# Kernel tuning notes

Measured on AMD Instinct MI355X. Metric: run time of the kernel, lower is better.

The kernel has to match this reference:

```python
import jax, jax.numpy as jnp
import numpy as np
import math

C = 512
TEXT_DIM = 768
HEADS = 8
HEAD_DIM = C // HEADS
GROUPS = 32
EPS = 1e-5


def setup_inputs() -> dict:
    key = jax.random.key(0)
    ks = jax.random.split(key, 12)
    B, H, W, T = 16, 64, 64, 77
    s = lambda fan_in: 1.0 / math.sqrt(fan_in)
    return {
        "x": jax.random.normal(ks[0], (B, C, H, W), jnp.float32),
        "text_emb": jax.random.normal(ks[1], (B, T, TEXT_DIM), jnp.float32),
        "gn_gamma": jnp.ones((C,), jnp.float32),
        "gn_beta": jnp.zeros((C,), jnp.float32),
        "q_w": jax.random.uniform(ks[2], (C, C), jnp.float32, -s(C), s(C)),
        "q_b": jax.random.uniform(ks[3], (C,), jnp.float32, -s(C), s(C)),
        "k_w": jax.random.uniform(ks[4], (C, TEXT_DIM), jnp.float32, -s(TEXT_DIM), s(TEXT_DIM)),
        "k_b": jax.random.uniform(ks[5], (C,), jnp.float32, -s(TEXT_DIM), s(TEXT_DIM)),
        "v_w": jax.random.uniform(ks[6], (C, TEXT_DIM), jnp.float32, -s(TEXT_DIM), s(TEXT_DIM)),
        "v_b": jax.random.uniform(ks[7], (C,), jnp.float32, -s(TEXT_DIM), s(TEXT_DIM)),
        "proj_w": jax.random.uniform(ks[8], (C, C), jnp.float32, -s(C), s(C)),
        "proj_b": jax.random.uniform(ks[9], (C,), jnp.float32, -s(C), s(C)),
    }


def _group_norm(x, gamma, beta):
    b, c, h, w = x.shape
    xg = x.reshape(b, GROUPS, c // GROUPS, h, w)
    mu = jnp.mean(xg, axis=(2, 3, 4), keepdims=True)
    var = jnp.var(xg, axis=(2, 3, 4), keepdims=True)
    xg = (xg - mu) * jax.lax.rsqrt(var + EPS)
    return xg.reshape(b, c, h, w) * gamma[None, :, None, None] + beta[None, :, None, None]


def reference(x, text_emb, gn_gamma, gn_beta, q_w, q_b, k_w, k_b, v_w, v_b, proj_w, proj_b):
    b, c, h, w = x.shape
    residual = x
    xn = _group_norm(x, gn_gamma, gn_beta)
    # 1x1 conv Q: [b,c,h,w] -> [b,c,h,w]
    q = jnp.einsum('bchw,oc->bohw', xn, q_w) + q_b[None, :, None, None]
    q = q.reshape(b, HEADS, HEAD_DIM, h * w)                  # [b,hd,dh,hw]
    # K,V linear then RAW reshape (matches torch's view semantics exactly)
    k = (jnp.einsum('btf,cf->btc', text_emb, k_w) + k_b).reshape(b, HEADS, HEAD_DIM, -1)
    v = (jnp.einsum('btf,cf->btc', text_emb, v_w) + v_b).reshape(b, HEADS, HEAD_DIM, -1)
    scale = 1.0 / math.sqrt(HEAD_DIM)
    attn = jax.nn.softmax(jnp.einsum('bhds,bhdt->bhst', q, k) * scale, axis=-1)
    out = jnp.einsum('bhst,bhdt->bhds', attn, v)              # [b,hd,dh,hw]
    out = out.reshape(b, c, h, w)
    out = jnp.einsum('bchw,oc->bohw', out, proj_w) + proj_b[None, :, None, None]
    return out + residual
```

## Files before the change

### kernel.cpp

```cpp
#include <hip/hip_runtime.h>

typedef unsigned short USHORT;
typedef __attribute__((ext_vector_type(8))) short short8;
typedef __attribute__((ext_vector_type(4))) float f32x4;

#define NB   16
#define NC   512
#define NHW  4096
#define NT   77
#define NF   768
#define NHEAD 8
#define NDH  64
#define TPAD 80
#define TPAD2 96
#define PSTR 104
#define BKS  64

__device__ __forceinline__ USHORT f2bf(float f){
  unsigned u = __builtin_bit_cast(unsigned, f);
  u += 0x7fffu + ((u >> 16) & 1u);
  return (USHORT)(u >> 16);
}
__device__ __forceinline__ unsigned pack2(float a, float b){
  return (unsigned)f2bf(a) | ((unsigned)f2bf(b) << 16);
}

__device__ __forceinline__ void gload16(const void* g, void* l){
  __builtin_amdgcn_global_load_lds((const __attribute__((address_space(1))) unsigned*)g,
                                   (__attribute__((address_space(3))) unsigned*)l, 16, 0, 0);
}

__device__ __forceinline__ int xcd_swz32(int x){ return ((x & 7) << 2) | (x >> 3); }

__global__ __launch_bounds__(256) void cvt_all_kernel(const float* __restrict__ s0, USHORT* __restrict__ d0, int n0,
                                                      const float* __restrict__ s1, USHORT* __restrict__ d1, int n1,
                                                      const float* __restrict__ s2, USHORT* __restrict__ d2, int n2,
                                                      const float* __restrict__ s3, USHORT* __restrict__ d3, int n3,
                                                      const float* __restrict__ s4, USHORT* __restrict__ d4, int n4){
  int i = blockIdx.x * 256 + threadIdx.x;
  const float* s; USHORT* d;
  if (i < n0){ s = s0; d = d0; }
  else { i -= n0;
    if (i < n1){ s = s1; d = d1; }
    else { i -= n1;
      if (i < n2){ s = s2; d = d2; }
      else { i -= n2;
        if (i < n3){ s = s3; d = d3; }
        else { i -= n3;
          if (i >= n4) return;
          s = s4; d = d4; } } } }
  float4 v = ((const float4*)s)[i];
  uint2 pk; pk.x = pack2(v.x, v.y); pk.y = pack2(v.z, v.w);
  ((uint2*)d)[i] = pk;
}

__global__ __launch_bounds__(256) void gnstats_kernel(const float* __restrict__ x, float2* __restrict__ stats){
  int gid = blockIdx.x;
  const float4* p = (const float4*)(x + (size_t)gid * 65536);
  float s = 0.f, s2 = 0.f;
  for (int i = threadIdx.x; i < 16384; i += 256){
    float4 v = p[i];
    s  += v.x + v.y + v.z + v.w;
    s2 += v.x*v.x + v.y*v.y + v.z*v.z + v.w*v.w;
  }
  #pragma unroll
  for (int off = 32; off; off >>= 1){ s += __shfl_down(s, off); s2 += __shfl_down(s2, off); }
  __shared__ float red[8];
  int wv = threadIdx.x >> 6;
  if ((threadIdx.x & 63) == 0){ red[wv] = s; red[4 + wv] = s2; }
  __syncthreads();
  if (threadIdx.x == 0){
    float S  = red[0] + red[1] + red[2] + red[3];
    float S2 = red[4] + red[5] + red[6] + red[7];
    float mu = S * (1.0f / 65536.0f);
    float var = S2 * (1.0f / 65536.0f) - mu * mu;
    stats[gid] = make_float2(mu, 1.0f / sqrtf(var + 1e-5f));
  }
}

__global__ __launch_bounds__(256) void gnorm_tr_kernel(const float* __restrict__ x, const float2* __restrict__ stats,
                                                       const float* __restrict__ gamma, const float* __restrict__ beta,
                                                       USHORT* __restrict__ xnT){
  __shared__ float tile[64][65];
  int b = blockIdx.z, c0 = blockIdx.y * 64, s0 = blockIdx.x * 64;
  int col = threadIdx.x & 63;
  int row4 = threadIdx.x >> 6;
  const float* xp = x + ((size_t)b * NC + c0) * NHW + s0;
  #pragma unroll
  for (int i = 0; i < 16; i++){
    int r = i * 4 + row4;
    tile[r][col] = xp[(size_t)r * NHW + col];
  }
  __syncthreads();
  int c = c0 + col;
  int g = c >> 4;
  float2 st = stats[b * 32 + g];
  float ga = gamma[c], be = beta[c];
  USHORT* op = xnT + ((size_t)b * NHW + s0) * NC + c;
  #pragma unroll
  for (int i = 0; i < 16; i++){
    int s = i * 4 + row4;
    float v = (tile[col][s] - st.x) * st.y * ga + be;
    op[(size_t)s * NC] = f2bf(v);
  }
}

__device__ __forceinline__ void gemm128_core(const USHORT* __restrict__ A, const USHORT* __restrict__ B,
                                             int m0, size_t brow0, USHORT* Alds, USHORT* Blds,
                                             f32x4 (&acc)[4][4]){
  const int tid = threadIdx.x;
  const int lane = tid & 63, wave = tid >> 6;
  const int l15 = lane & 15, lg = lane >> 4;
  const int wm = wave >> 1, wn = wave & 1;
  const int srow = lane >> 3, sslot = lane & 7;

  #pragma unroll
  for (int i = 0; i < 4; i++)
    #pragma unroll
    for (int j = 0; j < 4; j++) acc[i][j] = f32x4{0.f, 0.f, 0.f, 0.f};

  for (int k0 = 0; k0 < 512; k0 += BKS){
    #pragma unroll
    for (int i = 0; i < 4; i++){
      const int r0 = wave * 32 + i * 8;
      const int row = r0 + srow;
      const int slot = sslot ^ (row & 7);
      gload16(A + (size_t)(m0 + row) * NC + k0 + slot * 8, Alds + r0 * BKS);
      gload16(B + brow0 + (size_t)row * NC + k0 + slot * 8, Blds + r0 * BKS);
    }
    __syncthreads();
    #pragma unroll
    for (int ks = 0; ks < 2; ks++){
      short8 af[4], bf[4];
      #pragma unroll
      for (int i = 0; i < 4; i++){
        const int row = wm * 64 + i * 16 + l15;
        af[i] = *(const short8*)(Alds + row * BKS + (((ks * 4 + lg) ^ (row & 7)) * 8));
      }
      #pragma unroll
      for (int j = 0; j < 4; j++){
        const int row = wn * 64 + j * 16 + l15;
        bf[j] = *(const short8*)(Blds + row * BKS + (((ks * 4 + lg) ^ (row & 7)) * 8));
      }
      #pragma unroll
      for (int i = 0; i < 4; i++)
        #pragma unroll
        for (int j = 0; j < 4; j++)
          acc[i][j] = __builtin_amdgcn_mfma_f32_16x16x32_bf16(af[i], bf[j], acc[i][j], 0, 0, 0);
    }
    __syncthreads();
  }
}

__global__ __launch_bounds__(256, 3) void qattn_kernel(const USHORT* __restrict__ Aw, const USHORT* __restrict__ Bx,
                                                       const float* __restrict__ bias,
                                                       const USHORT* __restrict__ kb, const USHORT* __restrict__ vb,
                                                       USHORT* __restrict__ attnT){
  __shared__ USHORT smem[26624];
  const int lane = threadIdx.x & 63, wave = threadIdx.x >> 6;
  const int l15 = lane & 15, lg = lane >> 4;
  const int b = blockIdx.z;
  const int xx = xcd_swz32(blockIdx.x);
  const int m0b = blockIdx.y * 128;
  const size_t brow0 = ((size_t)b * NHW + xx * 128) * NC;
  f32x4 acc[4][4];
  gemm128_core(Aw, Bx, m0b, brow0, smem, smem + 8192, acc);

  const int wm = wave >> 1, wn = wave & 1;
  const int h = blockIdx.y * 2 + wm;
  const int m0 = h * 64;
  const int s0 = xx * 128 + wn * 64;
  const size_t bh = (size_t)b * NHEAD + h;
  char* qt = (char*)(smem + wave * 6656);

  #pragma unroll
  for (int i = 0; i < 4; i++){
    const int dbase = i * 16 + lg * 4;
    float b0 = bias[m0 + dbase], b1 = bias[m0 + dbase + 1];
    float b2 = bias[m0 + dbase + 2], b3 = bias[m0 + dbase + 3];
    #pragma unroll
    for (int j = 0; j < 4; j++){
      const int s = j * 16 + l15;
      uint2 pk;
      pk.x = pack2(acc[i][j][0] + b0, acc[i][j][1] + b1);
      pk.y = pack2(acc[i][j][2] + b2, acc[i][j][3] + b3);
      *(uint2*)(qt + s * 128 + ((dbase * 2) ^ ((s & 7) << 4))) = pk;
    }
  }
  short8 aq[4][2];
  #pragma unroll
  for (int i = 0; i < 4; i++){
    const int s = i * 16 + l15;
    #pragma unroll
    for (int ks = 0; ks < 2; ks++)
      aq[i][ks] = *(const short8*)(qt + s * 128 + ((ks * 64 + lg * 16) ^ ((s & 7) << 4)));
  }

  USHORT* plds = (USHORT*)qt;
  uint4 z{0u, 0u, 0u, 0u};
  *(uint4*)(qt + lane * (PSTR * 2) + 160) = z;
  *(uint4*)(qt + lane * (PSTR * 2) + 176) = z;

  short8 bk[5][2];
  const USHORT* kp = kb + bh * TPAD * NDH;
  #pragma unroll
  for (int j = 0; j < 5; j++)
    #pragma unroll
    for (int ks = 0; ks < 2; ks++)
      bk[j][ks] = *(const short8*)(kp + (j * 16 + l15) * NDH + ks * 32 + lg * 8);

  f32x4 sacc[4][5];
  #pragma unroll
  for (int i = 0; i < 4; i++)
    #pragma unroll
    for (int j = 0; j < 5; j++) sacc[i][j] = f32x4{0.f, 0.f, 0.f, 0.f};
  #pragma unroll
  for (int ks = 0; ks < 2; ks++)
    #pragma unroll
    for (int i = 0; i < 4; i++)
      #pragma unroll
      for (int j = 0; j < 5; j++)
        sacc[i][j] = __builtin_amdgcn_mfma_f32_16x16x32_bf16(aq[i][ks], bk[j][ks], sacc[i][j], 0, 0, 0);

  const float scale = 0.125f;
  #pragma unroll
  for (int i = 0; i < 4; i++){
    float v[5][4], mx[4], sm[4];
    #pragma unroll
    for (int r = 0; r < 4; r++) mx[r] = -3.0e38f;
    #pragma unroll
    for (int j = 0; j < 5; j++)
      #pragma unroll
      for (int r = 0; r < 4; r++){
        float t = sacc[i][j][r] * scale;
        if (j == 4 && l15 >= 13) t = -3.0e38f;
        v[j][r] = t;
        mx[r] = fmaxf(mx[r], t);
      }
    #pragma unroll
    for (int r = 0; r < 4; r++)
      #pragma unroll
      for (int d = 1; d < 16; d <<= 1) mx[r] = fmaxf(mx[r], __shfl_xor(mx[r], d));
    #pragma unroll
    for (int r = 0; r < 4; r++) sm[r] = 0.f;
    #pragma unroll
    for (int j = 0; j < 5; j++)
      #pragma unroll
      for (int r = 0; r < 4; r++){
        float p = __expf(v[j][r] - mx[r]);
        v[j][r] = p;
        sm[r] += p;
      }
    #pragma unroll
    for (int r = 0; r < 4; r++)
      #pragma unroll
      for (int d = 1; d < 16; d <<= 1) sm[r] += __shfl_xor(sm[r], d);
    #pragma unroll
    for (int r = 0; r < 4; r++){
      float inv = 1.0f / sm[r];
      #pragma unroll
      for (int j = 0; j < 5; j++)
        plds[(i * 16 + lg * 4 + r) * PSTR + j * 16 + l15] = f2bf(v[j][r] * inv);
    }
  }

  f32x4 oacc[4][4];
  #pragma unroll
  for (int it = 0; it < 4; it++)
    #pragma unroll
    for (int jt = 0; jt < 4; jt++) oacc[it][jt] = f32x4{0.f, 0.f, 0.f, 0.f};
  const USHORT* vp = vb + bh * NDH * TPAD2;
  #pragma unroll
  for (int ks = 0; ks < 3; ks++){
    short8 av[4], bpv[4];
    #pragma unroll
    for (int it = 0; it < 4; it++)
      av[it] = *(const short8*)(vp + (it * 16 + l15) * TPAD2 + ks * 32 + lg * 8);
    #pragma unroll
    for (int jt = 0; jt < 4; jt++)
      bpv[jt] = *(const short8*)(plds + (jt * 16 + l15) * PSTR + ks * 32 + lg * 8);
    #pragma unroll
    for (int it = 0; it < 4; it++)
      #pragma unroll
      for (int jt = 0; jt < 4; jt++)
        oacc[it][jt] = __builtin_amdgcn_mfma_f32_16x16x32_bf16(av[it], bpv[jt], oacc[it][jt], 0, 0, 0);
  }

  USHORT* ob = attnT + ((size_t)b * NHW + s0) * NC + h * NDH;
  #pragma unroll
  for (int it = 0; it < 4; it++)
    #pragma unroll
    for (int jt = 0; jt < 4; jt++){
      const int sl = jt * 16 + l15;
      uint2 pk;
      pk.x = pack2(oacc[it][jt][0], oacc[it][jt][1]);
      pk.y = pack2(oacc[it][jt][2], oacc[it][jt][3]);
      *(uint2*)(ob + (size_t)sl * NC + it * 16 + lg * 4) = pk;
    }
}

__global__ __launch_bounds__(256, 3) void projgemm_kernel(const USHORT* __restrict__ Aw, const USHORT* __restrict__ Battn,
                                                          const float* __restrict__ bias, const float* __restrict__ xres,
                                                          float* __restrict__ out){
  __shared__ USHORT Alds[128 * BKS], Blds[128 * BKS];
  const int b = blockIdx.z;
  const int xx = xcd_swz32(blockIdx.x);
  const int m0b = blockIdx.y * 128;
  const size_t brow0 = ((size_t)b * NHW + xx * 128) * NC;
  f32x4 acc[4][4];
  gemm128_core(Aw, Battn, m0b, brow0, Alds, Blds, acc);

  const int lane = threadIdx.x & 63, wave = threadIdx.x >> 6;
  const int l15 = lane & 15, lg = lane >> 4;
  const int m0 = m0b + (wave >> 1) * 64;
  const int n0 = xx * 128 + (wave & 1) * 64;
  #pragma unroll
  for (int i = 0; i < 4; i++){
    const int ob = m0 + i * 16 + lg * 4;
    #pragma unroll
    for (int r = 0; r < 4; r++){
      const int oc = ob + r;
      const float bb = bias[oc];
      #pragma unroll
      for (int j = 0; j < 4; j++){
        const int s = n0 + j * 16 + l15;
        const size_t idx = ((size_t)b * NC + oc) * NHW + s;
        out[idx] = acc[i][j][r] + bb + xres[idx];
      }
    }
  }
}

template<int KLEN>
__device__ __forceinline__ void mfma_core(const USHORT* const (&ap)[4], const USHORT* const (&bp)[4],
                                          f32x4 (&acc)[4][4]){
  short8 a_c[4], b_c[4];
  #pragma unroll
  for (int i = 0; i < 4; i++){ a_c[i] = *(const short8*)ap[i]; b_c[i] = *(const short8*)bp[i]; }
  #pragma unroll 2
  for (int k0 = 0; k0 < KLEN; k0 += 32){
    short8 a_n[4], b_n[4];
    if (k0 + 32 < KLEN){
      #pragma unroll
      for (int i = 0; i < 4; i++){
        a_n[i] = *(const short8*)(ap[i] + k0 + 32);
        b_n[i] = *(const short8*)(bp[i] + k0 + 32);
      }
    }
    #pragma unroll
    for (int i = 0; i < 4; i++)
      #pragma unroll
      for (int j = 0; j < 4; j++)
        acc[i][j] = __builtin_amdgcn_mfma_f32_16x16x32_bf16(a_c[i], b_c[j], acc[i][j], 0, 0, 0);
    #pragma unroll
    for (int i = 0; i < 4; i++){ a_c[i] = a_n[i]; b_c[i] = b_n[i]; }
  }
}

__global__ __launch_bounds__(256, 2) void kvgemm_kernel(const USHORT* __restrict__ kw, const USHORT* __restrict__ vw,
                                                        const USHORT* __restrict__ Tx,
                                                        const float* __restrict__ kbias, const float* __restrict__ vbias,
                                                        USHORT* __restrict__ kdst, USHORT* __restrict__ vdst){
  const int lane = threadIdx.x & 63, wave = threadIdx.x >> 6;
  const int l15 = lane & 15, lg = lane >> 4;
  const int b = blockIdx.z;
  const int mode = blockIdx.y;
  const USHORT* Wt = mode ? vw : kw;
  const float* bias = mode ? vbias : kbias;
  USHORT* dst = mode ? vdst : kdst;
  const int m0 = (wave >> 1) * 64;
  const int n0 = blockIdx.x * 128 + (wave & 1) * 64;
  const USHORT* ap[4]; const USHORT* bp[4];
  #pragma unroll
  for (int i = 0; i < 4; i++){
    int r = m0 + i * 16 + l15; r = r > 76 ? 76 : r;
    ap[i] = Tx + ((size_t)b * NT + r) * NF + lg * 8;
  }
  #pragma unroll
  for (int i = 0; i < 4; i++) bp[i] = Wt + (size_t)(n0 + i * 16 + l15) * NF + lg * 8;
  f32x4 acc[4][4];
  #pragma unroll
  for (int i = 0; i < 4; i++)
    #pragma unroll
    for (int j = 0; j < 4; j++) acc[i][j] = f32x4{0.f, 0.f, 0.f, 0.f};
  mfma_core<NF>(ap, bp, acc);
  #pragma unroll
  for (int i = 0; i < 4; i++){
    const int tb = m0 + i * 16 + lg * 4;
    #pragma unroll
    for (int r = 0; r < 4; r++){
      const int t = tb + r;
      if (t < NT){
        #pragma unroll
        for (int j = 0; j < 4; j++){
          const int c = n0 + j * 16 + l15;
          float v = acc[i][j][r] + bias[c];
          int fi = t * NC + c;
          int hh = fi / 4928;
          int rem = fi - hh * 4928;
          int dd = rem / 77;
          int tt = rem - dd * 77;
          size_t bhh = (size_t)(b * NHEAD + hh);
          if (mode == 0) dst[(bhh * TPAD + tt) * NDH + dd] = f2bf(v);
          else           dst[(bhh * NDH + dd) * TPAD2 + tt] = f2bf(v);
        }
      }
    }
  }
}

extern "C" void kernel_launch(void* const* d_in, const int* in_sizes, int n_in,
                              void* d_out, int out_size, void* d_ws, size_t ws_size,
                              hipStream_t stream){
  const float* x    = (const float*)d_in[0];
  const float* text = (const float*)d_in[1];
  const float* gn_g = (const float*)d_in[2];
  const float* gn_b = (const float*)d_in[3];
  const float* q_w  = (const float*)d_in[4];
  const float* q_b  = (const float*)d_in[5];
  const float* k_w  = (const float*)d_in[6];
  const float* k_b  = (const float*)d_in[7];
  const float* v_w  = (const float*)d_in[8];
  const float* v_b  = (const float*)d_in[9];
  const float* p_w  = (const float*)d_in[10];
  const float* p_b  = (const float*)d_in[11];
  float* out = (float*)d_out;

  char* ws = (char*)d_ws;
  size_t off = 0;
  auto alloc = [&](size_t bytes){ size_t o = off; off = (off + bytes + 255) & ~(size_t)255; return o; };
  size_t o_stats = alloc(512 * 8);
  size_t o_qwb   = alloc((size_t)NC * NC * 2);
  size_t o_pwb   = alloc((size_t)NC * NC * 2);
  size_t o_kwb   = alloc((size_t)NC * NF * 2);
  size_t o_vwb   = alloc((size_t)NC * NF * 2);
  size_t o_txb   = alloc((size_t)NB * NT * NF * 2);
  size_t o_kb    = alloc((size_t)NB * NHEAD * TPAD * NDH * 2);
  size_t o_vb    = alloc((size_t)NB * NHEAD * NDH * TPAD2 * 2);
  size_t o_xnT   = alloc((size_t)NB * NHW * NC * 2);
  size_t o_attnT = alloc((size_t)NB * NHW * NC * 2);
  (void)ws_size; (void)in_sizes; (void)n_in; (void)out_size;

  float2* stats = (float2*)(ws + o_stats);
  USHORT* qwb = (USHORT*)(ws + o_qwb);
  USHORT* pwb = (USHORT*)(ws + o_pwb);
  USHORT* kwb = (USHORT*)(ws + o_kwb);
  USHORT* vwb = (USHORT*)(ws + o_vwb);
  USHORT* txb = (USHORT*)(ws + o_txb);
  USHORT* kbuf = (USHORT*)(ws + o_kb);
  USHORT* vbuf = (USHORT*)(ws + o_vb);
  USHORT* xnT = (USHORT*)(ws + o_xnT);
  USHORT* attnT = (USHORT*)(ws + o_attnT);

  const int n0 = (NC * NC) / 4, n1 = (NC * NC) / 4, n2 = (NC * NF) / 4, n3 = (NC * NF) / 4,
            n4 = (NB * NT * NF) / 4;
  const int ntot = n0 + n1 + n2 + n3 + n4;
  hipLaunchKernelGGL(cvt_all_kernel, dim3((ntot + 255) / 256), dim3(256), 0, stream,
                     q_w, qwb, n0, p_w, pwb, n1, k_w, kwb, n2, v_w, vwb, n3, text, txb, n4);

  hipLaunchKernelGGL(gnstats_kernel, dim3(512), dim3(256), 0, stream, x, stats);
  hipLaunchKernelGGL(gnorm_tr_kernel, dim3(64, 8, 16), dim3(256), 0, stream, x, stats, gn_g, gn_b, xnT);
  hipLaunchKernelGGL(kvgemm_kernel, dim3(4, 2, 16), dim3(256), 0, stream, kwb, vwb, txb, k_b, v_b, kbuf, vbuf);
  hipLaunchKernelGGL(qattn_kernel, dim3(32, 4, 16), dim3(256), 0, stream, qwb, xnT, q_b, kbuf, vbuf, attnT);
  hipLaunchKernelGGL(projgemm_kernel, dim3(32, 4, 16), dim3(256), 0, stream, pwb, attnT, p_b, x, out);
}
```

Baseline: 259.8 us.

## Rewrite groupnorm-transpose as per-group register transpose with vector loads/stores

Replaces the LDS-tiled 64x64 transpose with one 1024-thread block per (batch, group). Each thread loads float4 from 8 channels, transposes in registers and writes 16-byte packed bf16 stores, with gamma*rstd folded into one multiply. The block index is swizzled so consecutive blocks spread across the grid, likely to balance memory channels or XCDs. The aim is wider global accesses and no shared-memory round trip, at the cost of strided 16-byte writes (1 KB stride) per thread.

Result: slower. 296.1 us (+14.0%).

```diff
diff --git a/kernel.cpp b/kernel.cpp
--- a/kernel.cpp
+++ b/kernel.cpp
@@ -78,30 +78,48 @@
   }
 }
 
-__global__ __launch_bounds__(256) void gnorm_tr_kernel(const float* __restrict__ x, const float2* __restrict__ stats,
-                                                       const float* __restrict__ gamma, const float* __restrict__ beta,
-                                                       USHORT* __restrict__ xnT){
-  __shared__ float tile[64][65];
-  int b = blockIdx.z, c0 = blockIdx.y * 64, s0 = blockIdx.x * 64;
-  int col = threadIdx.x & 63;
-  int row4 = threadIdx.x >> 6;
-  const float* xp = x + ((size_t)b * NC + c0) * NHW + s0;
-  #pragma unroll
-  for (int i = 0; i < 16; i++){
-    int r = i * 4 + row4;
-    tile[r][col] = xp[(size_t)r * NHW + col];
-  }
-  __syncthreads();
-  int c = c0 + col;
-  int g = c >> 4;
-  float2 st = stats[b * 32 + g];
-  float ga = gamma[c], be = beta[c];
-  USHORT* op = xnT + ((size_t)b * NHW + s0) * NC + c;
-  #pragma unroll
-  for (int i = 0; i < 16; i++){
-    int s = i * 4 + row4;
-    float v = (tile[col][s] - st.x) * st.y * ga + be;
-    op[(size_t)s * NC] = f2bf(v);
+__global__ __launch_bounds__(1024) void gn_tr_kernel(const float* __restrict__ x,
+                                                     const float2* __restrict__ stats,
+                                                     const float* __restrict__ gamma,
+                                                     const float* __restrict__ beta,
+                                                     USHORT* __restrict__ xnT){
+  const int dsp = blockIdx.x;
+  const int o = (dsp >> 3) & 1;
+  const int p = (dsp >> 4) * 8 + (dsp & 7);
+  const int base = 2 * p + o;
+  const int b = base >> 5, g = base & 31;
+  const int t = threadIdx.x;
+
+  const float2 st = stats[b * 32 + g];
+  const float mu = st.x, rs = st.y;
+  const float* xg = x + ((size_t)b * NC + g * 16) * NHW + t * 4;
+  USHORT* ob = xnT + ((size_t)b * NHW + t * 4) * NC + g * 16;
+
+  for (int half = 0; half < 2; ++half){
+    const int cb = g * 16 + half * 8;
+    const float g0 = gamma[cb+0]*rs, g1 = gamma[cb+1]*rs, g2 = gamma[cb+2]*rs, g3 = gamma[cb+3]*rs;
+    const float g4 = gamma[cb+4]*rs, g5 = gamma[cb+5]*rs, g6 = gamma[cb+6]*rs, g7 = gamma[cb+7]*rs;
+    const float b0 = beta[cb+0], b1 = beta[cb+1], b2 = beta[cb+2], b3 = beta[cb+3];
+    const float b4 = beta[cb+4], b5 = beta[cb+5], b6 = beta[cb+6], b7 = beta[cb+7];
+    const float* xh = xg + (size_t)(half * 8) * NHW;
+    float4 v0 = *(const float4*)(xh + 0 * (size_t)NHW);
+    float4 v1 = *(const float4*)(xh + 1 * (size_t)NHW);
+    float4 v2 = *(const float4*)(xh + 2 * (size_t)NHW);
+    float4 v3 = *(const float4*)(xh + 3 * (size_t)NHW);
+    float4 v4 = *(const float4*)(xh + 4 * (size_t)NHW);
+    float4 v5 = *(const float4*)(xh + 5 * (size_t)NHW);
+    float4 v6 = *(const float4*)(xh + 6 * (size_t)NHW);
+    float4 v7 = *(const float4*)(xh + 7 * (size_t)NHW);
+    USHORT* oh = ob + half * 8;
+#define GN_EMIT(COMP, EIDX) { \
+    unsigned w0 = pack2((v0.COMP - mu) * g0 + b0, (v1.COMP - mu) * g1 + b1); \
+    unsigned w1 = pack2((v2.COMP - mu) * g2 + b2, (v3.COMP - mu) * g3 + b3); \
+    unsigned w2 = pack2((v4.COMP - mu) * g4 + b4, (v5.COMP - mu) * g5 + b5); \
+    unsigned w3 = pack2((v6.COMP - mu) * g6 + b6, (v7.COMP - mu) * g7 + b7); \
+    uint4 pk{w0, w1, w2, w3};                                                \
+    *(uint4*)(oh + (size_t)(EIDX) * NC) = pk; }
+    GN_EMIT(x, 0) GN_EMIT(y, 1) GN_EMIT(z, 2) GN_EMIT(w, 3)
+#undef GN_EMIT
   }
 }
 
@@ -459,7 +477,7 @@
                      q_w, qwb, n0, p_w, pwb, n1, k_w, kwb, n2, v_w, vwb, n3, text, txb, n4);
 
   hipLaunchKernelGGL(gnstats_kernel, dim3(512), dim3(256), 0, stream, x, stats);
-  hipLaunchKernelGGL(gnorm_tr_kernel, dim3(64, 8, 16), dim3(256), 0, stream, x, stats, gn_g, gn_b, xnT);
+  hipLaunchKernelGGL(gn_tr_kernel, dim3(512), dim3(1024), 0, stream, x, stats, gn_g, gn_b, xnT);
   hipLaunchKernelGGL(kvgemm_kernel, dim3(4, 2, 16), dim3(256), 0, stream, kwb, vwb, txb, k_b, v_b, kbuf, vbuf);
   hipLaunchKernelGGL(qattn_kernel, dim3(32, 4, 16), dim3(256), 0, stream, qwb, xnT, q_b, kbuf, vbuf, attnT);
   hipLaunchKernelGGL(projgemm_kernel, dim3(32, 4, 16), dim3(256), 0, stream, pwb, attnT, p_b, x, out);
```
